# Optimization experiments

Hardware: AMD Instinct MI355X
Metric: run time of the kernel (lower is better)

The kernel has to match this reference:

```python
import jax, jax.numpy as jnp
import numpy as np

NUM_K_HEADS = 16
NUM_V_HEADS = 32
DK = 128
DV = 128
KCONV = 4
EPS = 1e-6
KEY_DIM = NUM_K_HEADS * DK      # 2048
VALUE_DIM = NUM_V_HEADS * DV    # 4096
HIDDEN = 2048
T_TOKENS = 4096


def setup_inputs() -> dict:
    key = jax.random.key(0)
    ks = jax.random.split(key, 10)
    s = 0.02
    return {
        "hidden_states": jax.random.normal(ks[0], (T_TOKENS, HIDDEN), jnp.float32),
        "W_qkv": jax.random.normal(ks[1], (2 * KEY_DIM + VALUE_DIM, HIDDEN), jnp.float32) * s,
        "W_z": jax.random.normal(ks[2], (VALUE_DIM, HIDDEN), jnp.float32) * s,
        "W_b": jax.random.normal(ks[3], (NUM_V_HEADS, HIDDEN), jnp.float32) * s,
        "W_a": jax.random.normal(ks[4], (NUM_V_HEADS, HIDDEN), jnp.float32) * s,
        "conv_weight": jax.random.normal(ks[5], (2 * KEY_DIM + VALUE_DIM, KCONV), jnp.float32) * 0.2,
        "dt_bias": jnp.ones((NUM_V_HEADS,), jnp.float32),
        "A_log": jax.random.normal(ks[6], (NUM_V_HEADS,), jnp.float32) * 0.5,
        "norm_weight": jnp.ones((DV,), jnp.float32),
        "W_out": jax.random.normal(ks[7], (HIDDEN, VALUE_DIM), jnp.float32) * s,
    }


def _l2norm(x):
    return x * jax.lax.rsqrt(jnp.sum(x * x, axis=-1, keepdims=True) + 1e-6)


def _gdn_forward(hidden_states, W_qkv, W_z, W_b, W_a, conv_weight,
                 dt_bias, A_log, norm_weight, W_out):
    T = hidden_states.shape[0]
    # input projections
    mixed_qkv = hidden_states @ W_qkv.T                         # [T, 2K+V]
    z = (hidden_states @ W_z.T).reshape(T, NUM_V_HEADS, DV)     # gate
    b = hidden_states @ W_b.T                                   # [T, Hv]
    a = hidden_states @ W_a.T                                   # [T, Hv]

    # depthwise causal conv1d (kernel 4) + silu, no bias
    xp = jnp.pad(mixed_qkv, ((KCONV - 1, 0), (0, 0)))
    conv = sum(xp[i:i + T] * conv_weight[:, i] for i in range(KCONV))
    x = jax.nn.silu(conv)

    q = x[:, :KEY_DIM].reshape(T, NUM_K_HEADS, DK)
    k = x[:, KEY_DIM:2 * KEY_DIM].reshape(T, NUM_K_HEADS, DK)
    v = x[:, 2 * KEY_DIM:].reshape(T, NUM_V_HEADS, DV)

    rep = NUM_V_HEADS // NUM_K_HEADS  # grouped value attention: repeat q/k heads
    q = jnp.repeat(_l2norm(q), rep, axis=1)  # [T, Hv, DK]
    k = jnp.repeat(_l2norm(k), rep, axis=1)

    beta = jax.nn.sigmoid(b)                                   # [T, Hv]
    g = -jnp.exp(A_log) * jax.nn.softplus(a + dt_bias)         # [T, Hv] log-decay
    scale = DK ** -0.5

    def step(S, inp):
        qt, kt, vt, bt, gt = inp
        S = S * jnp.exp(gt)[:, None, None]                     # gated decay
        kv = jnp.einsum('hk,hkv->hv', kt, S)                   # memory readout
        delta = (vt - kv) * bt[:, None]                        # delta rule update
        S = S + jnp.einsum('hk,hv->hkv', kt, delta)
        ot = jnp.einsum('hk,hkv->hv', qt, S) * scale
        return S, ot

    S0 = jnp.zeros((NUM_V_HEADS, DK, DV), mixed_qkv.dtype)
    _, o = jax.lax.scan(step, S0, (q, k, v, beta, g))          # o: [T, Hv, DV]

    # gated RMSNorm (norm before gate)
    var = jnp.mean(o * o, axis=-1, keepdims=True)
    on = o * jax.lax.rsqrt(var + EPS) * norm_weight
    y = on * jax.nn.silu(z)

    return y.reshape(T, VALUE_DIM) @ W_out.T                   # [T, HIDDEN]


def reference(hidden_states, W_qkv, W_z, W_b, W_a, conv_weight,
              dt_bias, A_log, norm_weight, W_out):
    return _gdn_forward(hidden_states, W_qkv, W_z, W_b, W_a, conv_weight,
                        dt_bias, A_log, norm_weight, W_out)
```

## Files before the change

kernel.cpp:

```cpp
#include <hip/hip_runtime.h>
#include <cstdint>
#include <cstddef>

typedef __bf16 bf16_t;
typedef __bf16 bf16x8 __attribute__((ext_vector_type(8)));
typedef __bf16 bf16x4 __attribute__((ext_vector_type(4)));
typedef float floatx4 __attribute__((ext_vector_type(4)));

__device__ __forceinline__ void async16(const bf16_t* g, bf16_t* l) {
  __builtin_amdgcn_global_load_lds(
      (const __attribute__((address_space(1))) unsigned int*)g,
      (__attribute__((address_space(3))) unsigned int*)l, 16, 0, 0);
}

__device__ __forceinline__ void barrier_lds() {
  asm volatile("s_waitcnt lgkmcnt(0)\n\ts_barrier" ::: "memory");
}

__device__ __forceinline__ float siluf(float x) { return x / (1.f + __expf(-x)); }

#define MFMA16(a, b, c) __builtin_amdgcn_mfma_f32_16x16x32_bf16(a, b, c, 0, 0, 0)

__global__ __launch_bounds__(256) void k_cvt(const float* __restrict__ in,
                                             bf16_t* __restrict__ out, int n4) {
  int i = blockIdx.x * 256 + threadIdx.x;
  if (i >= n4) return;
  const float4 f = ((const float4*)in)[i];
  bf16x4 r;
  r[0] = (bf16_t)f.x; r[1] = (bf16_t)f.y; r[2] = (bf16_t)f.z; r[3] = (bf16_t)f.w;
  ((bf16x4*)out)[i] = r;
}

__global__ __launch_bounds__(256) void k_build_wba(const float* __restrict__ wb,
                                                   const float* __restrict__ wa,
                                                   bf16_t* __restrict__ out) {
  int i = blockIdx.x * 256 + threadIdx.x;
  int e = i * 4;
  int row = e >> 11;
  int col = e & 2047;
  float4 f = make_float4(0.f, 0.f, 0.f, 0.f);
  if (row < 32)      f = *(const float4*)&wb[row * 2048 + col];
  else if (row < 64) f = *(const float4*)&wa[(row - 32) * 2048 + col];
  bf16x4 r;
  r[0] = (bf16_t)f.x; r[1] = (bf16_t)f.y; r[2] = (bf16_t)f.z; r[3] = (bf16_t)f.w;
  *(bf16x4*)&out[e] = r;
}

template<bool OUT_BF16>
__global__ __launch_bounds__(256) void gemm_bt(const bf16_t* __restrict__ A,
                                               const bf16_t* __restrict__ B,
                                               void* __restrict__ Cout,
                                               int M, int N, int K) {
  __shared__ __align__(16) bf16_t As[4096];
  __shared__ __align__(16) bf16_t Bs[4096];
  const int tid  = threadIdx.x;
  const int lane = tid & 63;
  const int wave = tid >> 6;
  const int quad = lane >> 4;
  const int l16  = lane & 15;
  const int wr   = (wave >> 1) * 64;
  const int wc   = (wave & 1) * 64;
  const int m0   = blockIdx.y * 128;
  const int n0   = blockIdx.x * 128;
  const int ra   = tid >> 2;
  const int ca   = (tid & 3) * 8;

  const bf16_t* gA = A + (size_t)(m0 + ra) * K + ca;
  const bf16_t* gB = B + (size_t)(n0 + ra) * K + ca;
  bf16_t* lA = &As[tid * 8];
  bf16_t* lB = &Bs[tid * 8];

  floatx4 acc[4][4] = {};

  for (int k0 = 0; k0 < K; k0 += 32) {
    __syncthreads();
    async16(gA + k0, lA);
    async16(gA + k0 + (size_t)64 * K, lA + 2048);
    async16(gB + k0, lB);
    async16(gB + k0 + (size_t)64 * K, lB + 2048);
    __syncthreads();
    bf16x8 af[4], bfr[4];
#pragma unroll
    for (int i = 0; i < 4; ++i) {
      af[i]  = *(const bf16x8*)&As[(wr + i * 16 + l16) * 32 + quad * 8];
      bfr[i] = *(const bf16x8*)&Bs[(wc + i * 16 + l16) * 32 + quad * 8];
    }
#pragma unroll
    for (int mi = 0; mi < 4; ++mi)
#pragma unroll
      for (int ni = 0; ni < 4; ++ni)
        acc[mi][ni] = MFMA16(af[mi], bfr[ni], acc[mi][ni]);
  }

#pragma unroll
  for (int mi = 0; mi < 4; ++mi) {
#pragma unroll
    for (int ni = 0; ni < 4; ++ni) {
      const int row = m0 + wr + mi * 16 + quad * 4;
      const int col = n0 + wc + ni * 16 + l16;
#pragma unroll
      for (int r = 0; r < 4; ++r) {
        if (OUT_BF16)
          ((bf16_t*)Cout)[(size_t)(row + r) * N + col] = (bf16_t)acc[mi][ni][r];
        else
          ((float*)Cout)[(size_t)(row + r) * N + col] = acc[mi][ni][r];
      }
    }
  }
}

template<bool OUT_BF16>
__global__ __launch_bounds__(512, 1) void gemm256(const bf16_t* __restrict__ A,
                                                  const bf16_t* __restrict__ B,
                                                  void* __restrict__ Cout,
                                                  int M, int N, int K) {
  extern __shared__ __align__(16) bf16_t sm[];
  const int tid  = threadIdx.x;
  const int lane = tid & 63;
  const int wave = tid >> 6;
  const int quad = lane >> 4;
  const int l16  = lane & 15;
  const int wm   = wave >> 2;
  const int wn   = wave & 3;

  const int gx  = (int)gridDim.x;
  const int nwg = gx * (int)gridDim.y;
  const int id  = (int)blockIdx.y * gx + (int)blockIdx.x;
  const int cpx = nwg >> 3;
  const int sw  = (id & 7) * cpx + (id >> 3);
  const int m0  = (sw / gx) * 256;
  const int n0  = (sw % gx) * 256;

  const int lr    = lane >> 2;
  const int lslot = (lane & 3) ^ ((lane >> 3) & 3);
  const bf16_t* gA = A + (size_t)(m0 + wave * 32 + lr) * K + lslot * 8;
  const bf16_t* gB = B + (size_t)(n0 + wave * 32 + lr) * K + lslot * 8;
  const int ldsA0 = wave * 1024 + lane * 8;
  const int ldsB0 = 8192 + wave * 1024 + lane * 8;

#define STG_A(u, kt) {                                          \
    bf16_t* la = sm + (u) * 16384 + ldsA0;                      \
    const bf16_t* ga = gA + (size_t)(kt) * 32;                  \
    async16(ga, la);                                            \
    async16(ga + (size_t)16 * K, la + 512); }
#define STG_B(u, kt) {                                          \
    bf16_t* lb = sm + (u) * 16384 + ldsB0;                      \
    const bf16_t* gb = gB + (size_t)(kt) * 32;                  \
    async16(gb, lb);                                            \
    async16(gb + (size_t)16 * K, lb + 512); }

  int offA[8], offB[4];
#pragma unroll
  for (int i = 0; i < 8; ++i) {
    int ra = wm * 128 + i * 16 + l16;
    offA[i] = (ra * 32 + quad * 8) ^ (((ra >> 1) & 3) << 3);
  }
#pragma unroll
  for (int i = 0; i < 4; ++i) {
    int rb = wn * 64 + i * 16 + l16;
    offB[i] = 8192 + ((rb * 32 + quad * 8) ^ (((rb >> 1) & 3) << 3));
  }

  floatx4 acc[8][4] = {};
  const int KT = K >> 5;

  STG_A(0, 0); STG_B(0, 0);
  STG_A(1, 1); STG_B(1, 1);
  STG_A(2, 2); STG_B(2, 2);
  asm volatile("s_waitcnt vmcnt(8)" ::: "memory");
  asm volatile("s_barrier" ::: "memory");

  for (int U = 0; U < KT; ++U) {
    const int bu = U & 3;
    const bf16_t* sb = sm + bu * 16384;
    const int un = U + 3;
    const int tu = un & 3;
    bf16x8 af[4], bfr[4];

#pragma unroll
    for (int i = 0; i < 4; ++i) {
      af[i]  = *(const bf16x8*)&sb[offA[i]];
      bfr[i] = *(const bf16x8*)&sb[offB[i]];
    }
    if (un < KT) STG_A(tu, un);
    asm volatile("s_barrier" ::: "memory");
    __builtin_amdgcn_s_setprio(1);
#pragma unroll
    for (int mi = 0; mi < 4; ++mi)
#pragma unroll
      for (int ni = 0; ni < 4; ++ni)
        acc[mi][ni] = MFMA16(af[mi], bfr[ni], acc[mi][ni]);
    __builtin_amdgcn_s_setprio(0);
    asm volatile("s_barrier" ::: "memory");

#pragma unroll
    for (int i = 0; i < 4; ++i) af[i] = *(const bf16x8*)&sb[offA[4 + i]];
    if (un < KT) STG_B(tu, un);
    if (un < KT)         asm volatile("s_waitcnt vmcnt(8)" ::: "memory");
    else if (U + 2 < KT) asm volatile("s_waitcnt vmcnt(4)" ::: "memory");
    else                 asm volatile("s_waitcnt vmcnt(0)" ::: "memory");
    asm volatile("s_barrier" ::: "memory");
    __builtin_amdgcn_s_setprio(1);
#pragma unroll
    for (int mi = 0; mi < 4; ++mi)
#pragma unroll
      for (int ni = 0; ni < 4; ++ni)
        acc[4 + mi][ni] = MFMA16(af[mi], bfr[ni], acc[4 + mi][ni]);
    __builtin_amdgcn_s_setprio(0);
    asm volatile("s_barrier" ::: "memory");
  }
#undef STG_A
#undef STG_B

#pragma unroll
  for (int mi = 0; mi < 8; ++mi) {
#pragma unroll
    for (int ni = 0; ni < 4; ++ni) {
      const int row = m0 + wm * 128 + mi * 16 + quad * 4;
      const int col = n0 + wn * 64 + ni * 16 + l16;
#pragma unroll
      for (int r = 0; r < 4; ++r) {
        if (OUT_BF16)
          ((bf16_t*)Cout)[(size_t)(row + r) * N + col] = (bf16_t)acc[mi][ni][r];
        else
          ((float*)Cout)[(size_t)(row + r) * N + col] = acc[mi][ni][r];
      }
    }
  }
}

__global__ __launch_bounds__(256) void k_betag(const float* __restrict__ cba,
                                               const float* __restrict__ A_log,
                                               const float* __restrict__ dtb,
                                               float* __restrict__ beta_t,
                                               float* __restrict__ g_t) {
  int i = blockIdx.x * 256 + threadIdx.x;
  int t = i >> 5, h = i & 31;
  float b = cba[t * 128 + h];
  float a = cba[t * 128 + 32 + h];
  beta_t[h * 4096 + t] = 1.f / (1.f + __expf(-b));
  float x = a + dtb[h];
  float sp = (x > 20.f) ? x : log1pf(__expf(x));
  g_t[h * 4096 + t] = -__expf(A_log[h]) * sp;
}

__global__ __launch_bounds__(64) void k_conv(const bf16_t* __restrict__ mixed,
                                             const float* __restrict__ cw,
                                             bf16_t* __restrict__ qo,
                                             bf16_t* __restrict__ ko,
                                             bf16_t* __restrict__ vo) {
  const int grp = blockIdx.x;
  const int t0 = blockIdx.y * 8;
  const int l = threadIdx.x;
  const int c0 = grp * 128 + l;
  const int c1 = c0 + 64;
  const float4 w0 = *(const float4*)&cw[c0 * 4];
  const float4 w1 = *(const float4*)&cw[c1 * 4];
  float h0[3], h1[3];
#pragma unroll
  for (int j = 0; j < 3; ++j) {
    int tt = t0 - 3 + j;
    h0[j] = (tt >= 0) ? (float)mixed[(size_t)tt * 8192 + c0] : 0.f;
    h1[j] = (tt >= 0) ? (float)mixed[(size_t)tt * 8192 + c1] : 0.f;
  }
#pragma unroll
  for (int i = 0; i < 8; ++i) {
    const int t = t0 + i;
    float x0 = (float)mixed[(size_t)t * 8192 + c0];
    float x1 = (float)mixed[(size_t)t * 8192 + c1];
    float a0 = w0.x * h0[0] + w0.y * h0[1] + w0.z * h0[2] + w0.w * x0;
    float a1 = w1.x * h1[0] + w1.y * h1[1] + w1.z * h1[2] + w1.w * x1;
    h0[0] = h0[1]; h0[1] = h0[2]; h0[2] = x0;
    h1[0] = h1[1]; h1[1] = h1[2]; h1[2] = x1;
    float v0 = siluf(a0), v1 = siluf(a1);
    if (grp < 32) {
      float s = v0 * v0 + v1 * v1;
#pragma unroll
      for (int m = 1; m < 64; m <<= 1) s += __shfl_xor(s, m);
      float r = rsqrtf(s + 1e-6f);
      if (grp < 16) {
        bf16_t* q = qo + ((size_t)t * 16 + grp) * 128;
        q[l]      = (bf16_t)(v0 * r * 0.08838834764831845f);
        q[l + 64] = (bf16_t)(v1 * r * 0.08838834764831845f);
      } else {
        bf16_t* k = ko + ((size_t)t * 16 + grp - 16) * 128;
        k[l]      = (bf16_t)(v0 * r);
        k[l + 64] = (bf16_t)(v1 * r);
      }
    } else {
      bf16_t* v = vo + ((size_t)t * 32 + grp - 32) * 128;
      v[l]      = (bf16_t)v0;
      v[l + 64] = (bf16_t)v1;
    }
  }
}

__global__ __launch_bounds__(256, 2) void k_prep(
    const bf16_t* __restrict__ qg, const bf16_t* __restrict__ kg,
    const bf16_t* __restrict__ vg,
    const float* __restrict__ bb_t, const float* __restrict__ gb_t,
    bf16_t* __restrict__ Vt, bf16_t* __restrict__ Wlo, bf16_t* __restrict__ Whi,
    bf16_t* __restrict__ Mout, bf16_t* __restrict__ kt, float* __restrict__ smalls) {
  const int c = blockIdx.x >> 5;
  const int h = blockIdx.x & 31;
  const int kh = h >> 1;
  const int t0 = c * 64;
  const int tid = threadIdx.x, lane = tid & 63, wave = tid >> 6;
  const int quad = lane >> 4, l16 = lane & 15;

  __shared__ __align__(16) bf16_t lsKQ[2][64][136];
  __shared__ float lsC[64][68];
  __shared__ float lsG[64], lsA[64], lsSc[64], lsBeta[64];

  {
    const int r = tid >> 2, s0 = (tid & 3) * 32;
    const bf16_t* kr = kg + ((size_t)(t0 + r) * 16 + kh) * 128 + s0;
    const bf16_t* qr = qg + ((size_t)(t0 + r) * 16 + kh) * 128 + s0;
#pragma unroll
    for (int j = 0; j < 4; ++j) {
      *(uint4*)&lsKQ[0][r][s0 + j * 8] = *(const uint4*)&kr[j * 8];
      *(uint4*)&lsKQ[1][r][s0 + j * 8] = *(const uint4*)&qr[j * 8];
    }
  }
  if (wave == 0) {
    float gv = gb_t[(size_t)h * 4096 + t0 + lane];
#pragma unroll
    for (int off = 1; off < 64; off <<= 1) {
      float n = __shfl_up(gv, off);
      if (lane >= off) gv += n;
    }
    float GL = __shfl(gv, 63);
    lsG[lane] = gv;
    lsA[lane] = __expf(gv);
    lsSc[lane] = __expf(GL - gv);
    lsBeta[lane] = bb_t[(size_t)h * 4096 + t0 + lane];
  }
  __syncthreads();

  const int mr = (wave >> 1) * 32, nr = (wave & 1) * 32;
  floatx4 ak[2][2] = {}, aq[2][2] = {};
  if (wave != 1) {
#pragma unroll
    for (int ks = 0; ks < 4; ++ks) {
      bf16x8 yf[2], xk[2], xq[2];
#pragma unroll
      for (int i = 0; i < 2; ++i) {
        yf[i] = *(const bf16x8*)&lsKQ[0][nr + i * 16 + l16][ks * 32 + quad * 8];
        xk[i] = *(const bf16x8*)&lsKQ[0][mr + i * 16 + l16][ks * 32 + quad * 8];
        xq[i] = *(const bf16x8*)&lsKQ[1][mr + i * 16 + l16][ks * 32 + quad * 8];
      }
#pragma unroll
      for (int i = 0; i < 2; ++i)
#pragma unroll
        for (int j = 0; j < 2; ++j) {
          ak[i][j] = MFMA16(xk[i], yf[j], ak[i][j]);
          aq[i][j] = MFMA16(xq[i], yf[j], aq[i][j]);
        }
    }
  }
  bf16_t* Mb = Mout + (size_t)(h * 64 + c) * 4096;
#pragma unroll
  for (int i = 0; i < 2; ++i)
#pragma unroll
    for (int j = 0; j < 2; ++j)
#pragma unroll
      for (int r = 0; r < 4; ++r) {
        int t = mr + i * 16 + quad * 4 + r;
        int s = nr + j * 16 + l16;
        float e = __expf(lsG[t] - lsG[s]);
        float cv = (s < t) ? lsBeta[t] * e * ak[i][j][r] : 0.f;
        float mv = (s <= t) ? e * aq[i][j][r] : 0.f;
        if (wave != 1) lsC[t][s] = cv;
        Mb[t * 64 + s] = (bf16_t)mv;
      }
  __syncthreads();

  const int col = tid & 127;
  const bool isW = tid >= 128;
  float vals[64];
#pragma unroll
  for (int t = 0; t < 64; ++t) {
    float b;
    if (!isW) b = (float)vg[((size_t)(t0 + t) * 32 + h) * 128 + col];
    else      b = lsA[t] * (float)lsKQ[0][t][col];
    vals[t] = lsBeta[t] * b;
  }
#pragma unroll
  for (int t = 1; t < 64; ++t) {
    float acc = vals[t];
#pragma unroll
    for (int s4 = 0; s4 <= (t - 1) >> 2; ++s4) {
      float4 cv = *(const float4*)&lsC[t][s4 * 4];
      acc -= cv.x * vals[s4 * 4 + 0];
      acc -= cv.y * vals[s4 * 4 + 1];
      acc -= cv.z * vals[s4 * 4 + 2];
      acc -= cv.w * vals[s4 * 4 + 3];
    }
    vals[t] = acc;
  }

  if (!isW) {
    bf16_t* vd = Vt + (size_t)(h * 64 + c) * 8192 + (size_t)col * 64;
#pragma unroll
    for (int j = 0; j < 16; ++j) {
      bf16x4 p;
      p[0] = (bf16_t)vals[j * 4 + 0];
      p[1] = (bf16_t)vals[j * 4 + 1];
      p[2] = (bf16_t)vals[j * 4 + 2];
      p[3] = (bf16_t)vals[j * 4 + 3];
      *(bf16x4*)&vd[j * 4] = p;
    }
  } else {
#pragma unroll
    for (int t = 0; t < 64; ++t) vals[t] = -vals[t];
  }

  if ((h & 1) == 0) {
    const int dk = tid >> 1, sh = (tid & 1) * 32;
    bf16_t* kd = kt + (size_t)(c * 16 + kh) * 8192 + (size_t)dk * 64 + sh;
#pragma unroll
    for (int j4 = 0; j4 < 4; ++j4) {
      bf16x8 v;
#pragma unroll
      for (int e = 0; e < 8; ++e) v[e] = lsKQ[0][sh + j4 * 8 + e][dk];
      *(bf16x8*)&kd[j4 * 8] = v;
    }
  }
  if (tid < 64) {
    float* sm = smalls + (size_t)(h * 64 + c) * 128;
    sm[tid] = lsA[tid];
    sm[64 + tid] = lsSc[tid];
  }
  __syncthreads();

  bf16_t* lsT = &lsKQ[0][0][0];
  if (isW) {
#pragma unroll
    for (int t = 0; t < 64; ++t) lsT[t * 272 + tid] = (bf16_t)vals[t];
  }
  __syncthreads();

  {
    const int r = tid >> 2, part = tid & 3;
    const bf16_t* src = &lsT[r * 272 + 128 + part * 32];
    bf16_t* Wb = (h < 16 ? Wlo : Whi) + (size_t)((h & 15) * 64 + c) * 8192 + r * 128 + part * 32;
#pragma unroll
    for (int j = 0; j < 4; ++j)
      *(uint4*)&Wb[j * 8] = *(const uint4*)&src[j * 8];
  }
}

__global__ __launch_bounds__(256, 1) void k_chain(
    const bf16_t* __restrict__ qg, const bf16_t* __restrict__ VtT,
    const bf16_t* __restrict__ Wlo, const bf16_t* __restrict__ Whi,
    const bf16_t* __restrict__ Mg, const bf16_t* __restrict__ ktg,
    const float* __restrict__ smalls, bf16_t* __restrict__ o) {
  const int h = blockIdx.x & 31;
  const int dv0 = (blockIdx.x >> 5) * 32;
  const int kh = h >> 1;
  const int tid = threadIdx.x, lane = tid & 63, wave = tid >> 6;
  const int quad = lane >> 4, l16 = lane & 15;
  const int trow = wave * 16 + quad * 4;

  __shared__ __align__(16) bf16_t lsXT[32][72];
  __shared__ __align__(16) bf16_t lsXbT[32][72];
  __shared__ __align__(16) bf16_t lsS[32][136];

  const bf16_t* Wbase = (h < 16 ? Wlo : Whi) + (size_t)(h & 15) * 64 * 8192;
  const bf16_t* Vbase = VtT + (size_t)h * 64 * 8192;
  const bf16_t* Mbase = Mg + (size_t)h * 64 * 4096;
  const float*  Sbase = smalls + (size_t)h * 64 * 128;

  const bf16_t* pW = Wbase + (size_t)(wave * 16 + l16) * 128 + quad * 8;
  const bf16_t* pQ = qg + ((size_t)(wave * 16 + l16) * 16 + kh) * 128 + quad * 8;
  const bf16_t* pK = ktg + (size_t)kh * 8192 + (size_t)(wave * 16 + l16) * 64 + quad * 8;
  const bf16_t* pM = Mbase + (size_t)(wave * 16 + l16) * 64 + quad * 8;
  const bf16_t* pV = Vbase + (size_t)(dv0 + l16) * 64 + trow;
  const float*  pS = Sbase;

  floatx4 sacc[2][2] = {};
  for (int i = tid; i < 32 * 136; i += 256) (&lsS[0][0])[i] = (bf16_t)0.f;

  bf16x8 nW[4], nQ[4], nK[4], nM[2];
  bf16x4 nV[2];
  float4 nA, nSc;
  float nAL;
  {
#pragma unroll
    for (int ks = 0; ks < 4; ++ks) {
      nW[ks] = *(const bf16x8*)&pW[ks * 32];
      nQ[ks] = *(const bf16x8*)&pQ[ks * 32];
    }
    nK[0] = *(const bf16x8*)&pK[0];
    nK[1] = *(const bf16x8*)&pK[32];
    nK[2] = *(const bf16x8*)&pK[4096];
    nK[3] = *(const bf16x8*)&pK[4096 + 32];
    nM[0] = *(const bf16x8*)&pM[0];
    nM[1] = *(const bf16x8*)&pM[32];
#pragma unroll
    for (int tn = 0; tn < 2; ++tn) nV[tn] = *(const bf16x4*)&pV[tn * 1024];
    nA  = *(const float4*)&pS[trow];
    nSc = *(const float4*)&pS[64 + trow];
    nAL = pS[63];
    pW += 8192; pQ += 131072; pK += 131072; pM += 4096; pV += 8192; pS += 128;
  }
  __syncthreads();

  for (int cc = 0; cc < 64; ++cc) {
    const int t0 = cc * 64;
    bf16x8 cW[4], cQ[4], cK[4], cM[2];
    float cV[8];
    float4 cA = nA, cSc = nSc;
    float cAL = nAL;
#pragma unroll
    for (int ks = 0; ks < 4; ++ks) { cW[ks] = nW[ks]; cQ[ks] = nQ[ks]; cK[ks] = nK[ks]; }
    cM[0] = nM[0]; cM[1] = nM[1];
#pragma unroll
    for (int tn = 0; tn < 2; ++tn)
#pragma unroll
      for (int r = 0; r < 4; ++r) cV[tn * 4 + r] = (float)nV[tn][r];

    if (cc + 1 < 64) {
#pragma unroll
      for (int ks = 0; ks < 4; ++ks) {
        nW[ks] = *(const bf16x8*)&pW[ks * 32];
        nQ[ks] = *(const bf16x8*)&pQ[ks * 32];
      }
      nK[0] = *(const bf16x8*)&pK[0];
      nK[1] = *(const bf16x8*)&pK[32];
      nK[2] = *(const bf16x8*)&pK[4096];
      nK[3] = *(const bf16x8*)&pK[4096 + 32];
      nM[0] = *(const bf16x8*)&pM[0];
      nM[1] = *(const bf16x8*)&pM[32];
#pragma unroll
      for (int tn = 0; tn < 2; ++tn) nV[tn] = *(const bf16x4*)&pV[tn * 1024];
      nA  = *(const float4*)&pS[trow];
      nSc = *(const float4*)&pS[64 + trow];
      nAL = pS[63];
      pW += 8192; pQ += 131072; pK += 131072; pM += 4096; pV += 8192; pS += 128;
    }

    bf16x8 bS[4][2];
#pragma unroll
    for (int ks = 0; ks < 4; ++ks)
#pragma unroll
      for (int tn = 0; tn < 2; ++tn)
        bS[ks][tn] = *(const bf16x8*)&lsS[tn * 16 + l16][ks * 32 + quad * 8];
    floatx4 xacc[2];
#pragma unroll
    for (int tn = 0; tn < 2; ++tn)
#pragma unroll
      for (int r = 0; r < 4; ++r) xacc[tn][r] = cV[tn * 4 + r];
#pragma unroll
    for (int ks = 0; ks < 4; ++ks)
#pragma unroll
      for (int tn = 0; tn < 2; ++tn)
        xacc[tn] = MFMA16(cW[ks], bS[ks][tn], xacc[tn]);
#pragma unroll
    for (int tn = 0; tn < 2; ++tn) {
      bf16x4 px, pb;
#pragma unroll
      for (int r = 0; r < 4; ++r) {
        px[r] = (bf16_t)xacc[tn][r];
        pb[r] = (bf16_t)(xacc[tn][r] * ((const float*)&cSc)[r]);
      }
      *(bf16x4*)&lsXT[tn * 16 + l16][trow] = px;
      *(bf16x4*)&lsXbT[tn * 16 + l16][trow] = pb;
    }
    floatx4 qacc[2] = {};
#pragma unroll
    for (int ks = 0; ks < 4; ++ks)
#pragma unroll
      for (int tn = 0; tn < 2; ++tn)
        qacc[tn] = MFMA16(cQ[ks], bS[ks][tn], qacc[tn]);
#pragma unroll
    for (int tn = 0; tn < 2; ++tn)
#pragma unroll
      for (int r = 0; r < 4; ++r) qacc[tn][r] *= ((const float*)&cA)[r];
#pragma unroll
    for (int mh = 0; mh < 2; ++mh)
#pragma unroll
      for (int tn = 0; tn < 2; ++tn)
#pragma unroll
        for (int r = 0; r < 4; ++r) sacc[mh][tn][r] *= cAL;
    barrier_lds();

#pragma unroll
    for (int ks = 0; ks < 2; ++ks)
#pragma unroll
      for (int tn = 0; tn < 2; ++tn) {
        bf16x8 bX = *(const bf16x8*)&lsXT[tn * 16 + l16][ks * 32 + quad * 8];
        qacc[tn] = MFMA16(cM[ks], bX, qacc[tn]);
      }
#pragma unroll
    for (int tn = 0; tn < 2; ++tn)
#pragma unroll
      for (int r = 0; r < 4; ++r)
        o[((size_t)(t0 + trow + r) * 32 + h) * 128 + dv0 + tn * 16 + l16] =
            (bf16_t)qacc[tn][r];

#pragma unroll
    for (int ks = 0; ks < 2; ++ks) {
      bf16x8 bXb[2];
#pragma unroll
      for (int tn = 0; tn < 2; ++tn)
        bXb[tn] = *(const bf16x8*)&lsXbT[tn * 16 + l16][ks * 32 + quad * 8];
#pragma unroll
      for (int mh = 0; mh < 2; ++mh)
#pragma unroll
        for (int tn = 0; tn < 2; ++tn)
          sacc[mh][tn] = MFMA16(cK[mh * 2 + ks], bXb[tn], sacc[mh][tn]);
    }
#pragma unroll
    for (int mh = 0; mh < 2; ++mh)
#pragma unroll
      for (int tn = 0; tn < 2; ++tn) {
        bf16x4 ps;
#pragma unroll
        for (int r = 0; r < 4; ++r) ps[r] = (bf16_t)sacc[mh][tn][r];
        *(bf16x4*)&lsS[tn * 16 + l16][(wave + 4 * mh) * 16 + quad * 4] = ps;
      }
    barrier_lds();
  }
}

__global__ __launch_bounds__(256) void k_gate(const bf16_t* __restrict__ o,
                                              const bf16_t* __restrict__ z,
                                              const float* __restrict__ nw,
                                              bf16_t* __restrict__ y) {
  const int row = blockIdx.x * 4 + (threadIdx.x >> 6);
  const int l = threadIdx.x & 63;
  const bf16_t* orow = o + (size_t)row * 128;
  float o0 = (float)orow[l], o1 = (float)orow[l + 64];
  float s = o0 * o0 + o1 * o1;
#pragma unroll
  for (int m = 1; m < 64; m <<= 1) s += __shfl_xor(s, m);
  float r = rsqrtf(s * (1.f / 128.f) + 1e-6f);
  const bf16_t* zrow = z + (size_t)row * 128;
  float z0 = (float)zrow[l], z1 = (float)zrow[l + 64];
  bf16_t* yrow = y + (size_t)row * 128;
  yrow[l]      = (bf16_t)(o0 * r * nw[l] * siluf(z0));
  yrow[l + 64] = (bf16_t)(o1 * r * nw[l + 64] * siluf(z1));
}

extern "C" void kernel_launch(void* const* d_in, const int* in_sizes, int n_in,
                              void* d_out, int out_size, void* d_ws, size_t ws_size,
                              hipStream_t stream) {
  const float* hidden = (const float*)d_in[0];
  const float* W_qkv  = (const float*)d_in[1];
  const float* W_z    = (const float*)d_in[2];
  const float* W_b    = (const float*)d_in[3];
  const float* W_a    = (const float*)d_in[4];
  const float* conv_w = (const float*)d_in[5];
  const float* dt_b   = (const float*)d_in[6];
  const float* A_log  = (const float*)d_in[7];
  const float* norm_w = (const float*)d_in[8];
  const float* W_out  = (const float*)d_in[9];
  float* out = (float*)d_out;

  static int gemm_attr_done = 0;
  if (!gemm_attr_done) {
    hipFuncSetAttribute(reinterpret_cast<const void*>(&gemm256<true>),
                        hipFuncAttributeMaxDynamicSharedMemorySize, 131072);
    hipFuncSetAttribute(reinterpret_cast<const void*>(&gemm256<false>),
                        hipFuncAttributeMaxDynamicSharedMemorySize, 131072);
    gemm_attr_done = 1;
  }

  char* w = (char*)d_ws;
  const size_t MB = 1024 * 1024;
  bf16_t* hs    = (bf16_t*)(w + 0 * MB);
  bf16_t* Wlo   = hs;
  bf16_t* wqkv  = (bf16_t*)(w + 16 * MB);
  bf16_t* Vtb   = wqkv;
  bf16_t* ybuf  = wqkv;
  bf16_t* wz    = (bf16_t*)(w + 48 * MB);
  bf16_t* Whi   = wz;
  bf16_t* wout  = (bf16_t*)(w + 64 * MB);
  bf16_t* wba   = (bf16_t*)(w + 80 * MB);
  bf16_t* mixed = (bf16_t*)(w + 81 * MB);
  bf16_t* obuf  = mixed;
  bf16_t* Mbuf  = (bf16_t*)(w + 113 * MB);
  bf16_t* ktb   = (bf16_t*)(w + 129 * MB);
  bf16_t* zbuf  = (bf16_t*)(w + 145 * MB);
  float*  cba   = (float*)(w + 177 * MB);
  float*  smalls= cba;
  bf16_t* qb    = (bf16_t*)(w + 179 * MB);
  bf16_t* kb    = (bf16_t*)(w + 195 * MB);
  bf16_t* vb    = (bf16_t*)(w + 211 * MB);
  float*  betab = (float*)(w + 243 * MB);
  float*  gbuf  = (float*)(w + 243 * MB + 512 * 1024);

  k_cvt<<<8192, 256, 0, stream>>>(hidden, hs, 2097152);
  k_cvt<<<16384, 256, 0, stream>>>(W_qkv, wqkv, 4194304);
  k_cvt<<<8192, 256, 0, stream>>>(W_z, wz, 2097152);
  k_cvt<<<8192, 256, 0, stream>>>(W_out, wout, 2097152);
  k_build_wba<<<256, 256, 0, stream>>>(W_b, W_a, wba);

  gemm256<true><<<dim3(32, 16), 512, 131072, stream>>>(hs, wqkv, mixed, 4096, 8192, 2048);
  gemm256<true><<<dim3(16, 16), 512, 131072, stream>>>(hs, wz, zbuf, 4096, 4096, 2048);
  gemm_bt<false><<<dim3(1, 32), 256, 0, stream>>>(hs, wba, cba, 4096, 128, 2048);
  k_betag<<<512, 256, 0, stream>>>(cba, A_log, dt_b, betab, gbuf);

  k_conv<<<dim3(64, 512), 64, 0, stream>>>(mixed, conv_w, qb, kb, vb);

  k_prep<<<2048, 256, 0, stream>>>(qb, kb, vb, betab, gbuf,
                                   Vtb, Wlo, Whi, Mbuf, ktb, smalls);
  k_chain<<<128, 256, 0, stream>>>(qb, Vtb, Wlo, Whi, Mbuf, ktb, smalls, obuf);

  k_gate<<<32768, 256, 0, stream>>>(obuf, zbuf, norm_w, ybuf);
  gemm256<false><<<dim3(8, 16), 512, 131072, stream>>>(ybuf, wout, out, 4096, 2048, 4096);
}
```

Before: 873.0 us.

## Split chain kernel over narrower value slices and use 128-row tiles for output GEMM

The sequential chunk-recurrence kernel now gives each block 16 value columns instead of 32, which doubles the grid from 128 to 256 blocks so more of the GPU's compute units run the serial scan. The output projection GEMM is templated on tile height and now uses 128x256 tiles, giving 256 workgroups instead of 128 to fill the device. The cost is that each chain block reloads the same W, Q, K and M operands for half as much work, and the smaller GEMM tiles reuse each loaded operand less.

```diff
diff --git a/kernel.cpp b/kernel.cpp
--- a/kernel.cpp
+++ b/kernel.cpp
@@ -20,6 +20,7 @@
 __device__ __forceinline__ float siluf(float x) { return x / (1.f + __expf(-x)); }
 
 #define MFMA16(a, b, c) __builtin_amdgcn_mfma_f32_16x16x32_bf16(a, b, c, 0, 0, 0)
+#define WAITV(n) asm volatile("s_waitcnt vmcnt(" #n ")" ::: "memory")
 
 __global__ __launch_bounds__(256) void k_cvt(const float* __restrict__ in,
                                              bf16_t* __restrict__ out, int n4) {
@@ -109,12 +110,16 @@
   }
 }
 
-template<bool OUT_BF16>
-__global__ __launch_bounds__(512, 1) void gemm256(const bf16_t* __restrict__ A,
-                                                  const bf16_t* __restrict__ B,
-                                                  void* __restrict__ Cout,
-                                                  int M, int N, int K) {
+template<int MH, bool OUT_BF16>
+__global__ __launch_bounds__(512, 1) void gemm_big(const bf16_t* __restrict__ A,
+                                                   const bf16_t* __restrict__ B,
+                                                   void* __restrict__ Cout,
+                                                   int M, int N, int K) {
   extern __shared__ __align__(16) bf16_t sm[];
+  constexpr int BM    = MH * 128;
+  constexpr int MFRAG = MH * 4;
+  constexpr int HF    = MFRAG / 2;
+  constexpr int BUFE  = MH * 4096 + 8192;
   const int tid  = threadIdx.x;
   const int lane = tid & 63;
   const int wave = tid >> 6;
@@ -128,65 +133,64 @@
   const int id  = (int)blockIdx.y * gx + (int)blockIdx.x;
   const int cpx = nwg >> 3;
   const int sw  = (id & 7) * cpx + (id >> 3);
-  const int m0  = (sw / gx) * 256;
+  const int m0  = (sw / gx) * BM;
   const int n0  = (sw % gx) * 256;
 
   const int lr    = lane >> 2;
   const int lslot = (lane & 3) ^ ((lane >> 3) & 3);
-  const bf16_t* gA = A + (size_t)(m0 + wave * 32 + lr) * K + lslot * 8;
+  const bf16_t* gA = A + (size_t)(m0 + wave * (MH * 16) + lr) * K + lslot * 8;
   const bf16_t* gB = B + (size_t)(n0 + wave * 32 + lr) * K + lslot * 8;
-  const int ldsA0 = wave * 1024 + lane * 8;
-  const int ldsB0 = 8192 + wave * 1024 + lane * 8;
+  const int ldsA0 = wave * (MH * 512) + lane * 8;
+  const int ldsB0 = MH * 4096 + wave * 1024 + lane * 8;
 
 #define STG_A(u, kt) {                                          \
-    bf16_t* la = sm + (u) * 16384 + ldsA0;                      \
+    bf16_t* la = sm + (u) * BUFE + ldsA0;                       \
     const bf16_t* ga = gA + (size_t)(kt) * 32;                  \
     async16(ga, la);                                            \
-    async16(ga + (size_t)16 * K, la + 512); }
+    if constexpr (MH == 2) async16(ga + (size_t)16 * K, la + 512); }
 #define STG_B(u, kt) {                                          \
-    bf16_t* lb = sm + (u) * 16384 + ldsB0;                      \
+    bf16_t* lb = sm + (u) * BUFE + ldsB0;                       \
     const bf16_t* gb = gB + (size_t)(kt) * 32;                  \
     async16(gb, lb);                                            \
     async16(gb + (size_t)16 * K, lb + 512); }
 
-  int offA[8], offB[4];
-#pragma unroll
-  for (int i = 0; i < 8; ++i) {
-    int ra = wm * 128 + i * 16 + l16;
+  int offA[MFRAG], offB[4];
+#pragma unroll
+  for (int i = 0; i < MFRAG; ++i) {
+    int ra = wm * (MFRAG * 16) + i * 16 + l16;
     offA[i] = (ra * 32 + quad * 8) ^ (((ra >> 1) & 3) << 3);
   }
 #pragma unroll
   for (int i = 0; i < 4; ++i) {
     int rb = wn * 64 + i * 16 + l16;
-    offB[i] = 8192 + ((rb * 32 + quad * 8) ^ (((rb >> 1) & 3) << 3));
-  }
-
-  floatx4 acc[8][4] = {};
+    offB[i] = MH * 4096 + ((rb * 32 + quad * 8) ^ (((rb >> 1) & 3) << 3));
+  }
+
+  floatx4 acc[MFRAG][4] = {};
   const int KT = K >> 5;
 
   STG_A(0, 0); STG_B(0, 0);
   STG_A(1, 1); STG_B(1, 1);
   STG_A(2, 2); STG_B(2, 2);
-  asm volatile("s_waitcnt vmcnt(8)" ::: "memory");
+  if constexpr (MH == 2) WAITV(8); else WAITV(6);
   asm volatile("s_barrier" ::: "memory");
 
   for (int U = 0; U < KT; ++U) {
     const int bu = U & 3;
-    const bf16_t* sb = sm + bu * 16384;
+    const bf16_t* sb = sm + bu * BUFE;
     const int un = U + 3;
     const int tu = un & 3;
-    bf16x8 af[4], bfr[4];
-
-#pragma unroll
-    for (int i = 0; i < 4; ++i) {
-      af[i]  = *(const bf16x8*)&sb[offA[i]];
-      bfr[i] = *(const bf16x8*)&sb[offB[i]];
-    }
+    bf16x8 af[HF], bfr[4];
+
+#pragma unroll
+    for (int i = 0; i < HF; ++i) af[i] = *(const bf16x8*)&sb[offA[i]];
+#pragma unroll
+    for (int i = 0; i < 4; ++i) bfr[i] = *(const bf16x8*)&sb[offB[i]];
     if (un < KT) STG_A(tu, un);
     asm volatile("s_barrier" ::: "memory");
     __builtin_amdgcn_s_setprio(1);
 #pragma unroll
-    for (int mi = 0; mi < 4; ++mi)
+    for (int mi = 0; mi < HF; ++mi)
 #pragma unroll
       for (int ni = 0; ni < 4; ++ni)
         acc[mi][ni] = MFMA16(af[mi], bfr[ni], acc[mi][ni]);
@@ -194,18 +198,18 @@
     asm volatile("s_barrier" ::: "memory");
 
 #pragma unroll
-    for (int i = 0; i < 4; ++i) af[i] = *(const bf16x8*)&sb[offA[4 + i]];
+    for (int i = 0; i < HF; ++i) af[i] = *(const bf16x8*)&sb[offA[HF + i]];
     if (un < KT) STG_B(tu, un);
-    if (un < KT)         asm volatile("s_waitcnt vmcnt(8)" ::: "memory");
-    else if (U + 2 < KT) asm volatile("s_waitcnt vmcnt(4)" ::: "memory");
-    else                 asm volatile("s_waitcnt vmcnt(0)" ::: "memory");
+    if (un < KT)         { if constexpr (MH == 2) WAITV(8); else WAITV(6); }
+    else if (U + 2 < KT) { if constexpr (MH == 2) WAITV(4); else WAITV(3); }
+    else                 WAITV(0);
     asm volatile("s_barrier" ::: "memory");
     __builtin_amdgcn_s_setprio(1);
 #pragma unroll
-    for (int mi = 0; mi < 4; ++mi)
+    for (int mi = 0; mi < HF; ++mi)
 #pragma unroll
       for (int ni = 0; ni < 4; ++ni)
-        acc[4 + mi][ni] = MFMA16(af[mi], bfr[ni], acc[4 + mi][ni]);
+        acc[HF + mi][ni] = MFMA16(af[mi], bfr[ni], acc[HF + mi][ni]);
     __builtin_amdgcn_s_setprio(0);
     asm volatile("s_barrier" ::: "memory");
   }
@@ -213,10 +217,10 @@
 #undef STG_B
 
 #pragma unroll
-  for (int mi = 0; mi < 8; ++mi) {
+  for (int mi = 0; mi < MFRAG; ++mi) {
 #pragma unroll
     for (int ni = 0; ni < 4; ++ni) {
-      const int row = m0 + wm * 128 + mi * 16 + quad * 4;
+      const int row = m0 + wm * (MFRAG * 16) + mi * 16 + quad * 4;
       const int col = n0 + wn * 64 + ni * 16 + l16;
 #pragma unroll
       for (int r = 0; r < 4; ++r) {
@@ -456,15 +460,15 @@
     const bf16_t* __restrict__ Mg, const bf16_t* __restrict__ ktg,
     const float* __restrict__ smalls, bf16_t* __restrict__ o) {
   const int h = blockIdx.x & 31;
-  const int dv0 = (blockIdx.x >> 5) * 32;
+  const int dv0 = (blockIdx.x >> 5) * 16;
   const int kh = h >> 1;
   const int tid = threadIdx.x, lane = tid & 63, wave = tid >> 6;
   const int quad = lane >> 4, l16 = lane & 15;
   const int trow = wave * 16 + quad * 4;
 
-  __shared__ __align__(16) bf16_t lsXT[32][72];
-  __shared__ __align__(16) bf16_t lsXbT[32][72];
-  __shared__ __align__(16) bf16_t lsS[32][136];
+  __shared__ __align__(16) bf16_t lsXT[16][72];
+  __shared__ __align__(16) bf16_t lsXbT[16][72];
+  __shared__ __align__(16) bf16_t lsS[16][136];
 
   const bf16_t* Wbase = (h < 16 ? Wlo : Whi) + (size_t)(h & 15) * 64 * 8192;
   const bf16_t* Vbase = VtT + (size_t)h * 64 * 8192;
@@ -478,11 +482,11 @@
   const bf16_t* pV = Vbase + (size_t)(dv0 + l16) * 64 + trow;
   const float*  pS = Sbase;
 
-  floatx4 sacc[2][2] = {};
-  for (int i = tid; i < 32 * 136; i += 256) (&lsS[0][0])[i] = (bf16_t)0.f;
+  floatx4 sacc[2] = {};
+  for (int i = tid; i < 16 * 136; i += 256) (&lsS[0][0])[i] = (bf16_t)0.f;
 
   bf16x8 nW[4], nQ[4], nK[4], nM[2];
-  bf16x4 nV[2];
+  bf16x4 nV;
   float4 nA, nSc;
   float nAL;
   {
@@ -497,8 +501,7 @@
     nK[3] = *(const bf16x8*)&pK[4096 + 32];
     nM[0] = *(const bf16x8*)&pM[0];
     nM[1] = *(const bf16x8*)&pM[32];
-#pragma unroll
-    for (int tn = 0; tn < 2; ++tn) nV[tn] = *(const bf16x4*)&pV[tn * 1024];
+    nV = *(const bf16x4*)&pV[0];
     nA  = *(const float4*)&pS[trow];
     nSc = *(const float4*)&pS[64 + trow];
     nAL = pS[63];
@@ -509,16 +512,14 @@
   for (int cc = 0; cc < 64; ++cc) {
     const int t0 = cc * 64;
     bf16x8 cW[4], cQ[4], cK[4], cM[2];
-    float cV[8];
+    float cV[4];
     float4 cA = nA, cSc = nSc;
     float cAL = nAL;
 #pragma unroll
     for (int ks = 0; ks < 4; ++ks) { cW[ks] = nW[ks]; cQ[ks] = nQ[ks]; cK[ks] = nK[ks]; }
     cM[0] = nM[0]; cM[1] = nM[1];
 #pragma unroll
-    for (int tn = 0; tn < 2; ++tn)
-#pragma unroll
-      for (int r = 0; r < 4; ++r) cV[tn * 4 + r] = (float)nV[tn][r];
+    for (int r = 0; r < 4; ++r) cV[r] = (float)nV[r];
 
     if (cc + 1 < 64) {
 #pragma unroll
@@ -532,94 +533,68 @@
       nK[3] = *(const bf16x8*)&pK[4096 + 32];
       nM[0] = *(const bf16x8*)&pM[0];
       nM[1] = *(const bf16x8*)&pM[32];
-#pragma unroll
-      for (int tn = 0; tn < 2; ++tn) nV[tn] = *(const bf16x4*)&pV[tn * 1024];
+      nV = *(const bf16x4*)&pV[0];
       nA  = *(const float4*)&pS[trow];
       nSc = *(const float4*)&pS[64 + trow];
       nAL = pS[63];
       pW += 8192; pQ += 131072; pK += 131072; pM += 4096; pV += 8192; pS += 128;
     }
 
-    bf16x8 bS[4][2];
+    bf16x8 bS[4];
 #pragma unroll
     for (int ks = 0; ks < 4; ++ks)
-#pragma unroll
-      for (int tn = 0; tn < 2; ++tn)
-        bS[ks][tn] = *(const bf16x8*)&lsS[tn * 16 + l16][ks * 32 + quad * 8];
-    floatx4 xacc[2];
-#pragma unroll
-    for (int tn = 0; tn < 2; ++tn)
-#pragma unroll
-      for (int r = 0; r < 4; ++r) xacc[tn][r] = cV[tn * 4 + r];
+      bS[ks] = *(const bf16x8*)&lsS[l16][ks * 32 + quad * 8];
+    floatx4 xacc;
+#pragma unroll
+    for (int r = 0; r < 4; ++r) xacc[r] = cV[r];
 #pragma unroll
     for (int ks = 0; ks < 4; ++ks)
-#pragma unroll
-      for (int tn = 0; tn < 2; ++tn)
-        xacc[tn] = MFMA16(cW[ks], bS[ks][tn], xacc[tn]);
-#pragma unroll
-    for (int tn = 0; tn < 2; ++tn) {
+      xacc = MFMA16(cW[ks], bS[ks], xacc);
+    {
       bf16x4 px, pb;
 #pragma unroll
       for (int r = 0; r < 4; ++r) {
-        px[r] = (bf16_t)xacc[tn][r];
-        pb[r] = (bf16_t)(xacc[tn][r] * ((const float*)&cSc)[r]);
+        px[r] = (bf16_t)xacc[r];
+        pb[r] = (bf16_t)(xacc[r] * ((const float*)&cSc)[r]);
       }
-      *(bf16x4*)&lsXT[tn * 16 + l16][trow] = px;
-      *(bf16x4*)&lsXbT[tn * 16 + l16][trow] = pb;
-    }
-    floatx4 qacc[2] = {};
+      *(bf16x4*)&lsXT[l16][trow] = px;
+      *(bf16x4*)&lsXbT[l16][trow] = pb;
+    }
+    floatx4 qacc = {};
 #pragma unroll
     for (int ks = 0; ks < 4; ++ks)
-#pragma unroll
-      for (int tn = 0; tn < 2; ++tn)
-        qacc[tn] = MFMA16(cQ[ks], bS[ks][tn], qacc[tn]);
-#pragma unroll
-    for (int tn = 0; tn < 2; ++tn)
-#pragma unroll
-      for (int r = 0; r < 4; ++r) qacc[tn][r] *= ((const float*)&cA)[r];
+      qacc = MFMA16(cQ[ks], bS[ks], qacc);
+#pragma unroll
+    for (int r = 0; r < 4; ++r) qacc[r] *= ((const float*)&cA)[r];
 #pragma unroll
     for (int mh = 0; mh < 2; ++mh)
 #pragma unroll
-      for (int tn = 0; tn < 2; ++tn)
-#pragma unroll
-        for (int r = 0; r < 4; ++r) sacc[mh][tn][r] *= cAL;
+      for (int r = 0; r < 4; ++r) sacc[mh][r] *= cAL;
     barrier_lds();
 
 #pragma unroll
-    for (int ks = 0; ks < 2; ++ks)
-#pragma unroll
-      for (int tn = 0; tn < 2; ++tn) {
-        bf16x8 bX = *(const bf16x8*)&lsXT[tn * 16 + l16][ks * 32 + quad * 8];
-        qacc[tn] = MFMA16(cM[ks], bX, qacc[tn]);
-      }
-#pragma unroll
-    for (int tn = 0; tn < 2; ++tn)
-#pragma unroll
-      for (int r = 0; r < 4; ++r)
-        o[((size_t)(t0 + trow + r) * 32 + h) * 128 + dv0 + tn * 16 + l16] =
-            (bf16_t)qacc[tn][r];
-
-#pragma unroll
     for (int ks = 0; ks < 2; ++ks) {
-      bf16x8 bXb[2];
-#pragma unroll
-      for (int tn = 0; tn < 2; ++tn)
-        bXb[tn] = *(const bf16x8*)&lsXbT[tn * 16 + l16][ks * 32 + quad * 8];
+      bf16x8 bX = *(const bf16x8*)&lsXT[l16][ks * 32 + quad * 8];
+      qacc = MFMA16(cM[ks], bX, qacc);
+    }
+#pragma unroll
+    for (int r = 0; r < 4; ++r)
+      o[((size_t)(t0 + trow + r) * 32 + h) * 128 + dv0 + l16] = (bf16_t)qacc[r];
+
+#pragma unroll
+    for (int ks = 0; ks < 2; ++ks) {
+      bf16x8 bXb = *(const bf16x8*)&lsXbT[l16][ks * 32 + quad * 8];
 #pragma unroll
       for (int mh = 0; mh < 2; ++mh)
-#pragma unroll
-        for (int tn = 0; tn < 2; ++tn)
-          sacc[mh][tn] = MFMA16(cK[mh * 2 + ks], bXb[tn], sacc[mh][tn]);
-    }
-#pragma unroll
-    for (int mh = 0; mh < 2; ++mh)
-#pragma unroll
-      for (int tn = 0; tn < 2; ++tn) {
-        bf16x4 ps;
-#pragma unroll
-        for (int r = 0; r < 4; ++r) ps[r] = (bf16_t)sacc[mh][tn][r];
-        *(bf16x4*)&lsS[tn * 16 + l16][(wave + 4 * mh) * 16 + quad * 4] = ps;
-      }
+        sacc[mh] = MFMA16(cK[mh * 2 + ks], bXb, sacc[mh]);
+    }
+#pragma unroll
+    for (int mh = 0; mh < 2; ++mh) {
+      bf16x4 ps;
+#pragma unroll
+      for (int r = 0; r < 4; ++r) ps[r] = (bf16_t)sacc[mh][r];
+      *(bf16x4*)&lsS[l16][(wave + 4 * mh) * 16 + quad * 4] = ps;
+    }
     barrier_lds();
   }
 }
@@ -660,10 +635,10 @@
 
   static int gemm_attr_done = 0;
   if (!gemm_attr_done) {
-    hipFuncSetAttribute(reinterpret_cast<const void*>(&gemm256<true>),
+    hipFuncSetAttribute(reinterpret_cast<const void*>(&gemm_big<2, true>),
                         hipFuncAttributeMaxDynamicSharedMemorySize, 131072);
-    hipFuncSetAttribute(reinterpret_cast<const void*>(&gemm256<false>),
-                        hipFuncAttributeMaxDynamicSharedMemorySize, 131072);
+    hipFuncSetAttribute(reinterpret_cast<const void*>(&gemm_big<1, false>),
+                        hipFuncAttributeMaxDynamicSharedMemorySize, 98304);
     gemm_attr_done = 1;
   }
 
@@ -697,8 +672,8 @@
   k_cvt<<<8192, 256, 0, stream>>>(W_out, wout, 2097152);
   k_build_wba<<<256, 256, 0, stream>>>(W_b, W_a, wba);
 
-  gemm256<true><<<dim3(32, 16), 512, 131072, stream>>>(hs, wqkv, mixed, 4096, 8192, 2048);
-  gemm256<true><<<dim3(16, 16), 512, 131072, stream>>>(hs, wz, zbuf, 4096, 4096, 2048);
+  gemm_big<2, true><<<dim3(32, 16), 512, 131072, stream>>>(hs, wqkv, mixed, 4096, 8192, 2048);
+  gemm_big<2, true><<<dim3(16, 16), 512, 131072, stream>>>(hs, wz, zbuf, 4096, 4096, 2048);
   gemm_bt<false><<<dim3(1, 32), 256, 0, stream>>>(hs, wba, cba, 4096, 128, 2048);
   k_betag<<<512, 256, 0, stream>>>(cba, A_log, dt_b, betab, gbuf);
 
@@ -706,8 +681,8 @@
 
   k_prep<<<2048, 256, 0, stream>>>(qb, kb, vb, betab, gbuf,
                                    Vtb, Wlo, Whi, Mbuf, ktb, smalls);
-  k_chain<<<128, 256, 0, stream>>>(qb, Vtb, Wlo, Whi, Mbuf, ktb, smalls, obuf);
+  k_chain<<<256, 256, 0, stream>>>(qb, Vtb, Wlo, Whi, Mbuf, ktb, smalls, obuf);
 
   k_gate<<<32768, 256, 0, stream>>>(obuf, zbuf, norm_w, ybuf);
-  gemm256<false><<<dim3(8, 16), 512, 131072, stream>>>(ybuf, wout, out, 4096, 2048, 4096);
-}
+  gemm_big<1, false><<<dim3(8, 32), 512, 98304, stream>>>(ybuf, wout, out, 4096, 2048, 4096);
+}
```

New measurement: 829.1 us. 5.0% less time.
